# Kernel tuning notes

Measured on AMD Instinct MI355X. Metric: run time of the kernel, lower is better.

The kernel has to match this reference:

```python
import jax, jax.numpy as jnp
import numpy as np

EPSILON = 1e-4  # self.epsilon


def setup_inputs() -> dict:
    key = jax.random.key(0)
    ks = jax.random.split(key, 7)
    N, C_in, L = 32, 128, 512
    C_p, P, n_cls = 64, 2000, 200
    x = jax.random.normal(ks[0], (N, C_in, L), dtype=jnp.float32)
    W1 = jax.random.normal(ks[1], (C_p, C_in, 1), dtype=jnp.float32) * 0.05
    b1 = jnp.zeros((C_p,), dtype=jnp.float32)
    W2 = jax.random.normal(ks[2], (C_p, C_p, 1), dtype=jnp.float32) * 0.05
    b2 = jnp.zeros((C_p,), dtype=jnp.float32)
    prototype_vectors = jax.random.uniform(ks[3], (P, C_p, 1), dtype=jnp.float32)
    last_w = jax.random.normal(ks[4], (n_cls, P), dtype=jnp.float32) * 0.02
    return {"x": x, "W1": W1, "b1": b1, "W2": W2, "b2": b2,
            "prototype_vectors": prototype_vectors, "last_w": last_w}


def _forward(x, W1, b1, W2, b2, prototype_vectors, last_w):
    # add_on_layers: 1x1 conv1d -> relu -> 1x1 conv1d -> sigmoid
    h = jax.nn.relu(jnp.einsum('ncl,oc->nol', x, W1[:, :, 0]) + b1[None, :, None])
    f = jax.nn.sigmoid(jnp.einsum('ncl,oc->nol', h, W2[:, :, 0]) + b2[None, :, None])
    # _l2_convolution (prototype kernel length 1, stride 1):
    # x2_patch_sum via conv with all-ones filter == per-position channel sum of f^2
    x2_patch_sum = jnp.sum(f * f, axis=1, keepdims=True)          # [N,1,L]
    p2 = jnp.sum(prototype_vectors ** 2, axis=(1, 2))             # [P]
    xp = jnp.einsum('ncl,pc->npl', f, prototype_vectors[:, :, 0])  # [N,P,L]
    distances = jax.nn.relu(x2_patch_sum - 2.0 * xp + p2[None, :, None])
    # -max_pool(-d) over full length == min over L
    min_distances = jnp.min(distances, axis=2)                    # [N,P]
    prototype_activations = jnp.log((min_distances + 1.0) / (min_distances + EPSILON))
    logits = prototype_activations @ last_w.T                     # [N,num_classes]
    return logits, min_distances


def reference(x, W1, b1, W2, b2, prototype_vectors, last_w):
    return _forward(x, W1, b1, W2, b2, prototype_vectors, last_w)
```

## Files before the change

kernel.cpp:

```cpp
#include <hip/hip_runtime.h>
#include <hip/hip_fp16.h>
#include <math.h>

#define EPS 1e-4f
#define N_   32
#define CIN  128
#define L_   512
#define CP   64
#define P_   2000
#define NCLS 200

typedef __attribute__((ext_vector_type(8))) _Float16 f16x8;
typedef __attribute__((ext_vector_type(4))) float f32x4;

__device__ inline void gl_lds16(const void* g, void* l) {
    __builtin_amdgcn_global_load_lds(
        (const __attribute__((address_space(1))) unsigned int*)g,
        (__attribute__((address_space(3))) unsigned int*)l, 16, 0, 0);
}
__device__ inline unsigned int packh2(float a, float b) {
    unsigned int lo = __half_as_ushort(__float2half(a));
    unsigned int hi = __half_as_ushort(__float2half(b));
    return lo | (hi << 16);
}

__global__ __launch_bounds__(256) void k0_proto(const float* __restrict__ proto,
    const float* __restrict__ W1, const float* __restrict__ W2,
    unsigned short* __restrict__ ph, unsigned short* __restrict__ w1h,
    unsigned short* __restrict__ w2h, float* __restrict__ p2)
{
    const int tid = threadIdx.x;
    const int bx  = blockIdx.x;
    if (bx == 500) {
        #pragma unroll
        for (int i = 0; i < 32; ++i) {
            int idx = i*256 + tid;
            w1h[idx] = __half_as_ushort(__float2half(W1[idx]));
        }
        return;
    }
    if (bx == 501) {
        #pragma unroll
        for (int i = 0; i < 16; ++i) {
            int idx = i*256 + tid;
            w2h[idx] = __half_as_ushort(__float2half(W2[idx]));
        }
        return;
    }
    const int p = bx*4 + (tid >> 6);
    const int k = tid & 63;
    float v = proto[(size_t)p*64 + k];
    ph[(size_t)p*64 + k] = __half_as_ushort(__float2half(v));
    float s = v*v;
    #pragma unroll
    for (int off = 32; off > 0; off >>= 1) s += __shfl_xor(s, off);
    if (k == 0) p2[p] = s;
}

__global__ __launch_bounds__(256) void k1_conv(const float* __restrict__ x,
    const unsigned short* __restrict__ w1h, const float* __restrict__ b1,
    const unsigned short* __restrict__ w2h, const float* __restrict__ b2,
    unsigned short* __restrict__ fT, float* __restrict__ x2buf)
{
    __shared__ float xS[128*32];
    __shared__ __align__(16) unsigned short hb[32*72];
    __shared__ float x2p[2][32];

    const int tid  = threadIdx.x;
    const int lane = tid & 63;
    const int wv   = tid >> 6;
    const int n    = blockIdx.y;
    const int lg   = blockIdx.x;

    {
        const float* xbase = x + (size_t)n*CIN*L_ + lg*32;
        #pragma unroll
        for (int i = 0; i < 4; ++i) {
            int blk = wv*4 + i;
            const float* src = xbase + (size_t)(blk*8 + (lane >> 3))*L_ + (lane & 7)*4;
            gl_lds16(src, &xS[blk*256]);
        }
    }
    __syncthreads();

    const int r  = lane & 15;
    const int g  = lane >> 4;
    const int lt = wv & 1;
    const int oh = wv >> 1;
    const int lrow = lt*16 + r;

    f32x4 acc[2];
    #pragma unroll
    for (int o2 = 0; o2 < 2; ++o2)
        acc[o2] = *(const f32x4*)(b1 + (oh*2 + o2)*16 + g*4);

    #pragma unroll
    for (int ks = 0; ks < 4; ++ks) {
        f16x8 B;
        #pragma unroll
        for (int i = 0; i < 8; ++i)
            B[i] = (_Float16)xS[(ks*32 + g*8 + i)*32 + lrow];
        #pragma unroll
        for (int o2 = 0; o2 < 2; ++o2) {
            int ot = oh*2 + o2;
            f16x8 A = *(const f16x8*)(w1h + (ot*16 + r)*128 + ks*32 + g*8);
            acc[o2] = __builtin_amdgcn_mfma_f32_16x16x32_f16(A, B, acc[o2], 0, 0, 0);
        }
    }
    #pragma unroll
    for (int o2 = 0; o2 < 2; ++o2) {
        int ot = oh*2 + o2;
        float v0 = fmaxf(acc[o2][0], 0.f), v1 = fmaxf(acc[o2][1], 0.f);
        float v2 = fmaxf(acc[o2][2], 0.f), v3 = fmaxf(acc[o2][3], 0.f);
        uint2 w2v = make_uint2(packh2(v0, v1), packh2(v2, v3));
        *(uint2*)((char*)hb + lrow*144 + ot*32 + g*8) = w2v;
    }
    __syncthreads();

    f32x4 acc2[2];
    #pragma unroll
    for (int o2 = 0; o2 < 2; ++o2)
        acc2[o2] = *(const f32x4*)(b2 + (oh*2 + o2)*16 + g*4);

    #pragma unroll
    for (int ks = 0; ks < 2; ++ks) {
        f16x8 B = *(const f16x8*)((const char*)hb + lrow*144 + ks*64 + g*16);
        #pragma unroll
        for (int o2 = 0; o2 < 2; ++o2) {
            int ot = oh*2 + o2;
            f16x8 A = *(const f16x8*)(w2h + (ot*16 + r)*64 + ks*32 + g*8);
            acc2[o2] = __builtin_amdgcn_mfma_f32_16x16x32_f16(A, B, acc2[o2], 0, 0, 0);
        }
    }

    char* gb = (char*)xS;
    float s = 0.f;
    float fv[2][4];
    #pragma unroll
    for (int o2 = 0; o2 < 2; ++o2)
        #pragma unroll
        for (int j = 0; j < 4; ++j) {
            float v = 1.f/(1.f + expf(-acc2[o2][j]));
            fv[o2][j] = v;
            s = fmaf(v, v, s);
        }
    s += __shfl_xor(s, 16);
    s += __shfl_xor(s, 32);
    if (lane < 16) x2p[oh][lrow] = s;

    #pragma unroll
    for (int o2 = 0; o2 < 2; ++o2) {
        int ot = oh*2 + o2;
        uint2 w2v = make_uint2(packh2(fv[o2][0], fv[o2][1]), packh2(fv[o2][2], fv[o2][3]));
        *(uint2*)(gb + lrow*144 + ot*32 + g*8) = w2v;
    }
    __syncthreads();

    {
        int l = tid >> 3, u = tid & 7;
        uint4 v = *(const uint4*)(gb + l*144 + u*16);
        ((uint4*)fT)[((size_t)(n*L_ + lg*32 + l))*8 + u] = v;
    }
    if (tid < 32)
        x2buf[n*L_ + lg*32 + tid] = x2p[0][tid] + x2p[1][tid];
}

__global__ __launch_bounds__(256) void k2_dist(
    const unsigned short* __restrict__ fT, const unsigned short* __restrict__ ph,
    const float* __restrict__ x2buf, float* __restrict__ md_part)
{
    __shared__ unsigned short fB[4096];
    __shared__ float x2S[64];

    const int tid  = threadIdx.x;
    const int lane = tid & 63;
    const int wv   = tid >> 6;
    const int n    = blockIdx.y;
    const int lg   = blockIdx.x >> 2;
    const int pg   = blockIdx.x & 3;

    {
        const char* gH = (const char*)(fT + ((size_t)n*L_ + lg*64)*CP);
        #pragma unroll
        for (int j = 0; j < 2; ++j) {
            int d  = tid*32 + j*16;
            int lr = d >> 7;
            int bo = d & 127;
            int pb = (lr << 7) + (bo ^ ((lr & 7) << 4));
            *(uint4*)((char*)fB + pb) = *(const uint4*)(gH + d);
        }
    }
    if (tid < 64) x2S[tid] = x2buf[n*L_ + lg*64 + tid];
    __syncthreads();

    const int g  = lane >> 4;
    const int pr = lane & 15;

    f16x8 af[4][2];
    #pragma unroll
    for (int lt = 0; lt < 4; ++lt) {
        int lrow = lt*16 + pr;
        #pragma unroll
        for (int ks = 0; ks < 2; ++ks) {
            int bo = (ks*64 + g*16) ^ ((lrow & 7) << 4);
            af[lt][ks] = *(const f16x8*)((const char*)fB + lrow*128 + bo);
        }
    }
    float4 xv[4];
    #pragma unroll
    for (int lt = 0; lt < 4; ++lt)
        xv[lt] = *(const float4*)&x2S[lt*16 + g*4];

    float* mp = md_part + ((size_t)lg*N_ + n)*P_;

    const int t0 = pg + 4*wv;
    f16x8 b[2], nb[2];
    {
        const int p = t0*16 + pr;
        #pragma unroll
        for (int ks = 0; ks < 2; ++ks)
            b[ks] = *(const f16x8*)(ph + (size_t)p*64 + ks*32 + g*8);
    }
    for (int t = t0; t < P_/16; t += 16) {
        const int tn = t + 16;
        if (tn < P_/16) {
            const int p = tn*16 + pr;
            #pragma unroll
            for (int ks = 0; ks < 2; ++ks)
                nb[ks] = *(const f16x8*)(ph + (size_t)p*64 + ks*32 + g*8);
        }

        float cm0 = 3.0e38f, cm1 = 3.0e38f, cm2 = 3.0e38f, cm3 = 3.0e38f;
        #pragma unroll
        for (int lt = 0; lt < 4; ++lt) {
            f32x4 c = {0.f, 0.f, 0.f, 0.f};
            c = __builtin_amdgcn_mfma_f32_16x16x32_f16(af[lt][0], b[0], c, 0, 0, 0);
            c = __builtin_amdgcn_mfma_f32_16x16x32_f16(af[lt][1], b[1], c, 0, 0, 0);
            cm0 = fminf(cm0, fmaf(-2.f, c[0], xv[lt].x));
            cm1 = fminf(cm1, fmaf(-2.f, c[1], xv[lt].y));
            cm2 = fminf(cm2, fmaf(-2.f, c[2], xv[lt].z));
            cm3 = fminf(cm3, fmaf(-2.f, c[3], xv[lt].w));
        }
        float v = fminf(fminf(cm0, cm1), fminf(cm2, cm3));
        v = fminf(v, __shfl_xor(v, 16));
        v = fminf(v, __shfl_xor(v, 32));
        if (lane < 16) mp[t*16 + lane] = v;

        b[0] = nb[0]; b[1] = nb[1];
    }
}

__global__ __launch_bounds__(256) void k2b_reduce(const float* __restrict__ md_part,
    const float* __restrict__ p2, float* __restrict__ md_out, float* __restrict__ acts)
{
    const int p = blockIdx.x*256 + threadIdx.x;
    const int n = blockIdx.y;
    if (p < P_) {
        float mv = 3.0e38f;
        #pragma unroll
        for (int lg = 0; lg < 8; ++lg)
            mv = fminf(mv, md_part[((size_t)lg*N_ + n)*P_ + p]);
        float m = fmaxf(mv + p2[p], 0.0f);
        md_out[n*P_ + p] = m;
        acts[n*P_ + p]   = logf((m + 1.0f) / (m + EPS));
    }
}

__global__ __launch_bounds__(256) void k3_logits(const float* __restrict__ acts,
    const float* __restrict__ last_w, float* __restrict__ out)
{
    const int wid  = (blockIdx.x * 256 + threadIdx.x) >> 6;
    const int lane = threadIdx.x & 63;
    const int n    = wid / NCLS;
    const int cls  = wid - n * NCLS;

    const float4* a = (const float4*)(acts + (size_t)n*P_);
    const float4* w = (const float4*)(last_w + (size_t)cls*P_);

    float acc = 0.f;
    #pragma unroll
    for (int it = 0; it < 8; ++it) {
        int idx = it*64 + lane;
        if (idx < P_/4) {
            float4 av = a[idx]; float4 wv = w[idx];
            acc += av.x*wv.x + av.y*wv.y + av.z*wv.z + av.w*wv.w;
        }
    }
    #pragma unroll
    for (int off = 32; off > 0; off >>= 1)
        acc += __shfl_down(acc, off);
    if (lane == 0)
        out[n*NCLS + cls] = acc;
}

extern "C" void kernel_launch(void* const* d_in, const int* in_sizes, int n_in,
                              void* d_out, int out_size, void* d_ws, size_t ws_size,
                              hipStream_t stream)
{
    const float* x      = (const float*)d_in[0];
    const float* W1     = (const float*)d_in[1];
    const float* b1     = (const float*)d_in[2];
    const float* W2     = (const float*)d_in[3];
    const float* b2     = (const float*)d_in[4];
    const float* proto  = (const float*)d_in[5];
    const float* last_w = (const float*)d_in[6];

    float* out = (float*)d_out;

    unsigned short* fT = (unsigned short*)d_ws;
    float* x2buf = (float*)(fT + (size_t)N_*L_*CP);
    float* acts  = x2buf + (size_t)N_*L_;
    unsigned short* ph = (unsigned short*)(acts + (size_t)N_*P_);
    float* p2      = (float*)(ph + (size_t)P_*CP);
    float* md_part = p2 + P_;
    unsigned short* w1h = (unsigned short*)(md_part + (size_t)8*N_*P_);
    unsigned short* w2h = w1h + 64*128;

    k0_proto  <<<502,           256, 0, stream>>>(proto, W1, W2, ph, w1h, w2h, p2);
    k1_conv   <<<dim3(16, 32),  256, 0, stream>>>(x, w1h, b1, w2h, b2, fT, x2buf);
    k2_dist   <<<dim3(32, 32),  256, 0, stream>>>(fT, ph, x2buf, md_part);
    k2b_reduce<<<dim3(8, 32),   256, 0, stream>>>(md_part, p2, out + N_*NCLS, acts);
    k3_logits <<<1600,          256, 0, stream>>>(acts, last_w, out);
}
```

Measured before the change: 34.68 us.

## Use bf16 activations and weights for logits GEMV; deepen prototype prefetch

Converts last_w to bf16 in the preprocessing kernel and stores prototype activations as bf16, so the logits kernel reads half the bytes and unpacks pairs with shifts and FMAs. Separately, the distance kernel now prefetches prototype fragments two iterations ahead instead of one, to hide global load latency. The bf16 path lowers precision of the logits, and the last_w conversion adds roughly 200 blocks to k0 on every call.

```diff
diff --git a/kernel.cpp b/kernel.cpp
--- a/kernel.cpp
+++ b/kernel.cpp
@@ -23,14 +23,39 @@
     unsigned int hi = __half_as_ushort(__float2half(b));
     return lo | (hi << 16);
 }
+__device__ inline unsigned short f2bf_rne(float f) {
+    unsigned int u = __float_as_uint(f);
+    unsigned int r = u + 0x7FFFu + ((u >> 16) & 1u);
+    return (unsigned short)(r >> 16);
+}
+__device__ inline float bfdot2(unsigned a, unsigned b, float acc) {
+    float a0 = __uint_as_float(a << 16);
+    float a1 = __uint_as_float(a & 0xFFFF0000u);
+    float b0 = __uint_as_float(b << 16);
+    float b1 = __uint_as_float(b & 0xFFFF0000u);
+    return fmaf(a1, b1, fmaf(a0, b0, acc));
+}
 
 __global__ __launch_bounds__(256) void k0_proto(const float* __restrict__ proto,
     const float* __restrict__ W1, const float* __restrict__ W2,
+    const float* __restrict__ last_w,
     unsigned short* __restrict__ ph, unsigned short* __restrict__ w1h,
-    unsigned short* __restrict__ w2h, float* __restrict__ p2)
+    unsigned short* __restrict__ w2h, unsigned short* __restrict__ lwB,
+    float* __restrict__ p2)
 {
     const int tid = threadIdx.x;
     const int bx  = blockIdx.x;
+    if (bx >= 502) {
+        int idx8 = (bx - 502)*256 + tid;
+        if (idx8 < 50000) {
+            const float4* src = (const float4*)(last_w + (size_t)idx8*8);
+            float4 v0 = src[0], v1 = src[1];
+            unsigned short o[8] = { f2bf_rne(v0.x), f2bf_rne(v0.y), f2bf_rne(v0.z), f2bf_rne(v0.w),
+                                    f2bf_rne(v1.x), f2bf_rne(v1.y), f2bf_rne(v1.z), f2bf_rne(v1.w) };
+            *(uint4*)(lwB + (size_t)idx8*8) = *(const uint4*)o;
+        }
+        return;
+    }
     if (bx == 500) {
         #pragma unroll
         for (int i = 0; i < 32; ++i) {
@@ -214,28 +239,34 @@
     float* mp = md_part + ((size_t)lg*N_ + n)*P_;
 
     const int t0 = pg + 4*wv;
-    f16x8 b[2], nb[2];
+    f16x8 bA[2], bB[2], bC[2];
     {
         const int p = t0*16 + pr;
         #pragma unroll
         for (int ks = 0; ks < 2; ++ks)
-            b[ks] = *(const f16x8*)(ph + (size_t)p*64 + ks*32 + g*8);
+            bA[ks] = *(const f16x8*)(ph + (size_t)p*64 + ks*32 + g*8);
+    }
+    if (t0 + 16 < P_/16) {
+        const int p = (t0+16)*16 + pr;
+        #pragma unroll
+        for (int ks = 0; ks < 2; ++ks)
+            bB[ks] = *(const f16x8*)(ph + (size_t)p*64 + ks*32 + g*8);
     }
     for (int t = t0; t < P_/16; t += 16) {
-        const int tn = t + 16;
-        if (tn < P_/16) {
-            const int p = tn*16 + pr;
+        const int t2 = t + 32;
+        if (t2 < P_/16) {
+            const int p = t2*16 + pr;
             #pragma unroll
             for (int ks = 0; ks < 2; ++ks)
-                nb[ks] = *(const f16x8*)(ph + (size_t)p*64 + ks*32 + g*8);
+                bC[ks] = *(const f16x8*)(ph + (size_t)p*64 + ks*32 + g*8);
         }
 
         float cm0 = 3.0e38f, cm1 = 3.0e38f, cm2 = 3.0e38f, cm3 = 3.0e38f;
         #pragma unroll
         for (int lt = 0; lt < 4; ++lt) {
             f32x4 c = {0.f, 0.f, 0.f, 0.f};
-            c = __builtin_amdgcn_mfma_f32_16x16x32_f16(af[lt][0], b[0], c, 0, 0, 0);
-            c = __builtin_amdgcn_mfma_f32_16x16x32_f16(af[lt][1], b[1], c, 0, 0, 0);
+            c = __builtin_amdgcn_mfma_f32_16x16x32_f16(af[lt][0], bA[0], c, 0, 0, 0);
+            c = __builtin_amdgcn_mfma_f32_16x16x32_f16(af[lt][1], bA[1], c, 0, 0, 0);
             cm0 = fminf(cm0, fmaf(-2.f, c[0], xv[lt].x));
             cm1 = fminf(cm1, fmaf(-2.f, c[1], xv[lt].y));
             cm2 = fminf(cm2, fmaf(-2.f, c[2], xv[lt].z));
@@ -246,12 +277,14 @@
         v = fminf(v, __shfl_xor(v, 32));
         if (lane < 16) mp[t*16 + lane] = v;
 
-        b[0] = nb[0]; b[1] = nb[1];
+        bA[0] = bB[0]; bA[1] = bB[1];
+        bB[0] = bC[0]; bB[1] = bC[1];
     }
 }
 
 __global__ __launch_bounds__(256) void k2b_reduce(const float* __restrict__ md_part,
-    const float* __restrict__ p2, float* __restrict__ md_out, float* __restrict__ acts)
+    const float* __restrict__ p2, float* __restrict__ md_out,
+    unsigned short* __restrict__ actsB)
 {
     const int p = blockIdx.x*256 + threadIdx.x;
     const int n = blockIdx.y;
@@ -262,28 +295,31 @@
             mv = fminf(mv, md_part[((size_t)lg*N_ + n)*P_ + p]);
         float m = fmaxf(mv + p2[p], 0.0f);
         md_out[n*P_ + p] = m;
-        acts[n*P_ + p]   = logf((m + 1.0f) / (m + EPS));
-    }
-}
-
-__global__ __launch_bounds__(256) void k3_logits(const float* __restrict__ acts,
-    const float* __restrict__ last_w, float* __restrict__ out)
+        actsB[(size_t)n*P_ + p] = f2bf_rne(logf((m + 1.0f) / (m + EPS)));
+    }
+}
+
+__global__ __launch_bounds__(256) void k3_logits(const unsigned short* __restrict__ actsB,
+    const unsigned short* __restrict__ lwB, float* __restrict__ out)
 {
     const int wid  = (blockIdx.x * 256 + threadIdx.x) >> 6;
     const int lane = threadIdx.x & 63;
     const int n    = wid / NCLS;
     const int cls  = wid - n * NCLS;
 
-    const float4* a = (const float4*)(acts + (size_t)n*P_);
-    const float4* w = (const float4*)(last_w + (size_t)cls*P_);
+    const uint4* a = (const uint4*)(actsB + (size_t)n*P_);
+    const uint4* w = (const uint4*)(lwB + (size_t)cls*P_);
 
     float acc = 0.f;
     #pragma unroll
-    for (int it = 0; it < 8; ++it) {
+    for (int it = 0; it < 4; ++it) {
         int idx = it*64 + lane;
-        if (idx < P_/4) {
-            float4 av = a[idx]; float4 wv = w[idx];
-            acc += av.x*wv.x + av.y*wv.y + av.z*wv.z + av.w*wv.w;
+        if (idx < P_/8) {
+            uint4 av = a[idx], wv = w[idx];
+            acc = bfdot2(av.x, wv.x, acc);
+            acc = bfdot2(av.y, wv.y, acc);
+            acc = bfdot2(av.z, wv.z, acc);
+            acc = bfdot2(av.w, wv.w, acc);
         }
     }
     #pragma unroll
@@ -309,16 +345,18 @@
 
     unsigned short* fT = (unsigned short*)d_ws;
     float* x2buf = (float*)(fT + (size_t)N_*L_*CP);
-    float* acts  = x2buf + (size_t)N_*L_;
-    unsigned short* ph = (unsigned short*)(acts + (size_t)N_*P_);
+    unsigned short* actsB = (unsigned short*)(x2buf + (size_t)N_*L_);
+    unsigned short* ph = actsB + (size_t)N_*P_;
     float* p2      = (float*)(ph + (size_t)P_*CP);
     float* md_part = p2 + P_;
     unsigned short* w1h = (unsigned short*)(md_part + (size_t)8*N_*P_);
-    unsigned short* w2h = w1h + 64*128;
-
-    k0_proto  <<<502,           256, 0, stream>>>(proto, W1, W2, ph, w1h, w2h, p2);
+    unsigned short* w2h = w1h + 64*CIN;
+    unsigned short* lwB = w2h + 64*CP;
+
+    k0_proto  <<<698,           256, 0, stream>>>(proto, W1, W2, last_w,
+                                                  ph, w1h, w2h, lwB, p2);
     k1_conv   <<<dim3(16, 32),  256, 0, stream>>>(x, w1h, b1, w2h, b2, fT, x2buf);
     k2_dist   <<<dim3(32, 32),  256, 0, stream>>>(fT, ph, x2buf, md_part);
-    k2b_reduce<<<dim3(8, 32),   256, 0, stream>>>(md_part, p2, out + N_*NCLS, acts);
-    k3_logits <<<1600,          256, 0, stream>>>(acts, last_w, out);
-}
+    k2b_reduce<<<dim3(8, 32),   256, 0, stream>>>(md_part, p2, out + N_*NCLS, actsB);
+    k3_logits <<<1600,          256, 0, stream>>>(actsB, lwB, out);
+}
```

New measurement: 35.17 us, median of 2. Within noise of the previous version (+1.4%).
